# Kernel tuning notes

Hardware: AMD Instinct MI355X
Metric: run time of the kernel (lower is better)

## Reference

```python
import jax, jax.numpy as jnp
import numpy as np

N_NODE = 50000
EMB = 128
LAYERS = 2
B = 1024
L = 50
E = 1_600_000


def setup_inputs() -> dict:
    key = jax.random.key(0)
    ks = jax.random.split(key, 21)
    d = EMB
    stdv = 1.0 / np.sqrt(d)
    u = lambda k, shape: jax.random.uniform(k, shape, minval=-stdv, maxval=stdv, dtype=jnp.float32)
    inp = {
        'adj_row': jax.random.randint(ks[0], (E,), 0, N_NODE, dtype=jnp.int32),
        'adj_col': jax.random.randint(ks[1], (E,), 0, N_NODE, dtype=jnp.int32),
        'adj_val': jax.random.uniform(ks[2], (E,), dtype=jnp.float32) / 32.0,  # ~row-normalized sparse adjacency
        'embedding': jax.random.normal(ks[3], (N_NODE, d), dtype=jnp.float32) * 0.1,
        'session_item': jax.random.randint(ks[4], (B, L), 0, N_NODE, dtype=jnp.int32),  # 0 hits the zero pad row
        'session_len': jnp.full((B, 1), float(L), dtype=jnp.float32),
        'D': jax.random.uniform(ks[5], (B, B), dtype=jnp.float32) / B,
        'A_sess': jax.random.uniform(ks[6], (B, B), dtype=jnp.float32) / B,
        'A_gnn': jax.random.uniform(ks[7], (B, L, 2 * L), dtype=jnp.float32) / L,
        'alias_pos': jax.random.randint(ks[8], (B, L), 0, L, dtype=jnp.int32),
        'hidden': jax.random.normal(ks[9], (B, L, d), dtype=jnp.float32) * 0.1,
        'W_in': u(ks[10], (d, d)), 'b_in': u(ks[11], (d,)),
        'W_out': u(ks[12], (d, d)), 'b_out': u(ks[13], (d,)),
        'w_ih': u(ks[14], (3 * d, 2 * d)), 'b_ih': u(ks[15], (3 * d,)),
        'w_hh': u(ks[16], (3 * d, d)), 'b_hh': u(ks[17], (3 * d,)),
        'b_iah': u(ks[18], (d,)), 'b_oah': u(ks[19], (d,)),
    }
    return inp


def reference(adj_row, adj_col, adj_val, embedding, session_item, session_len,
              D, A_sess, A_gnn, alias_pos, hidden,
              W_in, b_in, W_out, b_out, w_ih, b_ih, w_hh, b_hh, b_iah, b_oah):
    # ---- HyperConv: layers of sparse (COO) adjacency @ embedding, summed over hops ----
    emb = embedding
    final = embedding
    for _ in range(LAYERS):
        emb = jax.ops.segment_sum(adj_val[:, None] * emb[adj_col], adj_row, num_segments=N_NODE)
        final = final + emb
    item_emb = final  # [N_NODE, d]

    # ---- LineConv: zero-padded gather + mean pool over session, then session-graph propagation ----
    pad_table = jnp.concatenate([jnp.zeros((1, EMB), embedding.dtype), embedding], axis=0)
    seq_h = pad_table[session_item]                      # [B, L, d]
    sess = jnp.sum(seq_h, axis=1) / session_len          # [B, d]
    DA = D @ A_sess                                      # [B, B]
    acc = sess
    s = sess
    for _ in range(LAYERS):
        s = DA @ s
        acc = acc + s
    session_emb = acc                                    # [B, d]

    # ---- GNN: gather per-session in/out adjacency rows, gated GRU-style update ----
    in_out = jnp.take_along_axis(A_gnn, alias_pos[:, :, None], axis=1)  # [B, L, 2L]
    h_in = hidden @ W_in.T + b_in
    h_out = hidden @ W_out.T + b_out
    input_in = jnp.einsum('bij,bjd->bid', in_out[:, :, :L], h_in) + b_iah
    input_out = jnp.einsum('bij,bjd->bid', in_out[:, :, L:], h_out) + b_oah
    inputs = jnp.concatenate([input_in, input_out], axis=2)             # [B, L, 2d]
    gi = inputs @ w_ih.T + b_ih
    gh = hidden @ w_hh.T + b_hh
    i_r, i_i, i_n = jnp.split(gi, 3, axis=2)
    h_r, h_i, h_n = jnp.split(gh, 3, axis=2)
    resetgate = jax.nn.sigmoid(i_r + h_r)
    inputgate = jax.nn.sigmoid(i_i + h_i)
    newgate = jnp.tanh(i_n + resetgate * h_n)
    hy = newgate + inputgate * (hidden - newgate)        # [B, L, d]

    return item_emb, session_emb, hy
```

## Files before the change

### kernel.cpp

```cpp
#include <hip/hip_runtime.h>

#define EMB 128
#define NN 50000
#define BB 1024
#define LL 50
#define NBK 49
#define NEB 512
#define NCONV 2048

typedef float f32x4 __attribute__((ext_vector_type(4)));
typedef float f32x2 __attribute__((ext_vector_type(2)));
typedef unsigned short u16;
typedef unsigned int u32;
typedef unsigned long long u64;
typedef u16 u16x4 __attribute__((ext_vector_type(4)));
typedef u32 u32x4 __attribute__((ext_vector_type(4)));
typedef short bf16x8 __attribute__((ext_vector_type(8)));

__device__ __forceinline__ float u2f(u16 u) {
    union { unsigned int i; float f; } v; v.i = ((unsigned int)u) << 16; return v.f;
}
__device__ __forceinline__ u16 f2b(float f) {
    union { float f; unsigned int i; } v; v.f = f;
    unsigned int i = v.i;
    return (u16)((i + 0x7FFFu + ((i >> 16) & 1u)) >> 16);
}
__device__ __forceinline__ float lo2f(u32 w) { return u2f((u16)(w & 0xffffu)); }
__device__ __forceinline__ float hi2f(u32 w) { return u2f((u16)(w >> 16)); }
__device__ __forceinline__ float sigmoidf_(float x) { return 1.f / (1.f + __expf(-x)); }
__device__ __forceinline__ float tanhf_(float x) {
    float e = __expf(-2.f * x);
    return (1.f - e) / (1.f + e);
}

__global__ __launch_bounds__(256) void prep_kernel(
    const float* __restrict__ emb, const float* __restrict__ A, const float* __restrict__ D,
    const float* __restrict__ whh,
    u16* __restrict__ emb_bf, u16* __restrict__ A_bf, u16* __restrict__ D_bf,
    u16* __restrict__ whh_bf,
    const int* __restrict__ rowi, int* __restrict__ bcnt,
    const float* __restrict__ w_ih, const float* __restrict__ W_in, const float* __restrict__ W_out,
    const float* __restrict__ b_in, const float* __restrict__ b_out,
    const float* __restrict__ b_iah, const float* __restrict__ b_oah, const float* __restrict__ b_ih,
    u16* __restrict__ WcT_bf, float* __restrict__ u123,
    int E, int chunk)
{
    __shared__ int lc[NBK];
    __shared__ float wrow[256];
    __shared__ float red[3][256];
    int tid = threadIdx.x;

    if (blockIdx.x >= NCONV) {
        int d = blockIdx.x - NCONV;
        int c = tid;
        wrow[c] = w_ih[d * 256 + c];
        __syncthreads();
        const float* W = (c < 128) ? W_in : W_out;
        const float* wr = wrow + ((c < 128) ? 0 : 128);
        int cc = c & 127;
        float acc = 0.f;
#pragma unroll 4
        for (int j = 0; j < 128; j++) acc += wr[j] * W[j * 128 + cc];
        WcT_bf[d * 256 + c] = f2b(acc);
        float p1 = (c < 128) ? b_in[c] * wrow[c] : 0.f;
        float p2 = (c >= 128) ? b_out[cc] * wrow[c] : 0.f;
        float p3 = (c < 128) ? b_iah[c] * wrow[c] : b_oah[cc] * wrow[c];
        red[0][c] = p1; red[1][c] = p2; red[2][c] = p3;
        __syncthreads();
        for (int off = 128; off > 0; off >>= 1) {
            if (c < off) {
                red[0][c] += red[0][c + off];
                red[1][c] += red[1][c + off];
                red[2][c] += red[2][c + off];
            }
            __syncthreads();
        }
        if (c == 0) {
            u123[d] = red[0][0];
            u123[384 + d] = red[1][0];
            u123[768 + d] = red[2][0] + b_ih[d];
        }
        return;
    }

    int gid = blockIdx.x * 256 + tid;
    int stride = NCONV * 256;
    if (blockIdx.x < NEB) {
        if (tid < NBK) lc[tid] = 0;
        __syncthreads();
        int beg = blockIdx.x * chunk, end = min(E, beg + chunk);
        for (int e = beg + tid; e < end; e += 256)
            atomicAdd(&lc[rowi[e] >> 10], 1);
        __syncthreads();
        if (tid < NBK) bcnt[blockIdx.x * NBK + tid] = lc[tid];
    }
    for (int i = gid; i < 1600000; i += stride) {
        f32x4 v = *(const f32x4*)(emb + (size_t)i * 4);
        u16x4 p;
#pragma unroll
        for (int t = 0; t < 4; t++) p[t] = f2b(v[t]);
        *(u16x4*)(emb_bf + (size_t)i * 4) = p;
    }
    for (int i = gid; i < 2146304; i += stride) {
        const float* s; u16* d; int off;
        if (i < 1048576)      { s = A;   d = A_bf;   off = i; }
        else if (i < 2097152) { s = D;   d = D_bf;   off = i - 1048576; }
        else                  { s = whh; d = whh_bf; off = i - 2097152; }
        d[off] = f2b(s[off]);
    }
}

__global__ __launch_bounds__(512) void bktscan_kernel(
    const int* __restrict__ bcnt, int* __restrict__ sofs, int* __restrict__ btot)
{
    __shared__ int ps[512];
    int k = blockIdx.x, t = threadIdx.x;
    int c = bcnt[t * NBK + k];
    ps[t] = c; __syncthreads();
    for (int off = 1; off < 512; off <<= 1) {
        int v = (t >= off) ? ps[t - off] : 0;
        __syncthreads();
        ps[t] += v; __syncthreads();
    }
    sofs[t * NBK + k] = ps[t] - c;
    if (t == 511) btot[k] = ps[511];
}

__global__ __launch_bounds__(64) void btotal_kernel(
    const int* __restrict__ btot, int* __restrict__ bofs, int E)
{
    if (threadIdx.x == 0) {
        int run = 0;
        for (int k = 0; k < NBK; k++) { bofs[k] = run; run += btot[k]; }
        bofs[NBK] = E;
    }
}

__global__ __launch_bounds__(256) void emit_kernel(
    const int* __restrict__ rowi, const int* __restrict__ coli, const float* __restrict__ val,
    const int* __restrict__ sofs, const int* __restrict__ bofs,
    u64* __restrict__ egs, int E, int chunk)
{
    __shared__ int cur[NBK];
    int b = blockIdx.x, tid = threadIdx.x;
    if (tid < NBK) cur[tid] = bofs[tid] + sofs[b * NBK + tid];
    __syncthreads();
    int beg = b * chunk, end = min(E, beg + chunk);
    for (int e = beg + tid; e < end; e += 256) {
        int r = rowi[e];
        int slot = atomicAdd(&cur[r >> 10], 1);
        u64 entry = ((u64)(u32)(r & 1023) << 32)
                  | (u64)((u32)(u16)coli[e] | ((u32)f2b(val[e]) << 16));
        egs[slot] = entry;
    }
}

__global__ __launch_bounds__(1024) void binsort2_kernel(
    const u64* __restrict__ egs, const int* __restrict__ bofs,
    int* __restrict__ row_ptr, u32* __restrict__ eg, int E)
{
    __shared__ int cnt_s[1024];
    __shared__ int ps[1024];
    int k = blockIdx.x, tid = threadIdx.x;
    int r0 = k << 10;
    int beg = bofs[k], end = bofs[k + 1];
    cnt_s[tid] = 0;
    __syncthreads();
    for (int i = beg + tid; i < end; i += 1024)
        atomicAdd(&cnt_s[(int)(egs[i] >> 32)], 1);
    __syncthreads();
    int v = cnt_s[tid];
    ps[tid] = v; __syncthreads();
    for (int off = 1; off < 1024; off <<= 1) {
        int t = (tid >= off) ? ps[tid - off] : 0;
        __syncthreads();
        ps[tid] += t; __syncthreads();
    }
    int ex = beg + ps[tid] - v;
    if (r0 + tid <= NN) row_ptr[r0 + tid] = ex;
    if (k == NBK - 1 && tid == 1023) row_ptr[NN] = E;
    cnt_s[tid] = ex;
    __syncthreads();
    for (int i = beg + tid; i < end; i += 1024) {
        u64 entry = egs[i];
        int rlo = (int)(entry >> 32);
        int p = atomicAdd(&cnt_s[rlo], 1);
        eg[p] = (u32)entry;
    }
}

template<int FUSE>
__global__ __launch_bounds__(256) void gatherb_kernel(
    const int* __restrict__ row_ptr, const u32* __restrict__ eg,
    const u16* __restrict__ src, const float* __restrict__ emb0,
    u16* __restrict__ dst_bf, float* __restrict__ dst_f)
{
    int wave = threadIdx.x >> 6;
    int lane = threadIdx.x & 63;
    int g  = lane >> 4;
    int fl = lane & 15;
    int r = blockIdx.x * 4 + wave;
    if (r >= NN) return;
    int beg = row_ptr[r], end = row_ptr[r + 1];

    float acc[8];
#pragma unroll
    for (int t = 0; t < 8; t++) acc[t] = 0.f;

    if (beg < end) {
        int last = end - 1;
        int npair = (end - beg + 7) >> 3;
        u32 pkA = eg[min(beg + g, last)];
        u32 pkB = eg[min(beg + 4 + g, last)];
        float vA = (beg + g     < end) ? u2f((u16)(pkA >> 16)) : 0.f;
        float vB = (beg + 4 + g < end) ? u2f((u16)(pkB >> 16)) : 0.f;
        u32x4 xA = *(const u32x4*)(src + ((pkA & 0xffffu) << 7) + (fl << 3));
        u32x4 xB = *(const u32x4*)(src + ((pkB & 0xffffu) << 7) + (fl << 3));
        pkA = eg[min(beg + 8  + g, last)];
        pkB = eg[min(beg + 12 + g, last)];

        int e = beg;
        for (int p = 0; p < npair; p++) {
            float cvA = vA, cvB = vB;
            u32x4 cxA = xA, cxB = xB;
            int eN = e + 8;
            vA = (eN + g     < end) ? u2f((u16)(pkA >> 16)) : 0.f;
            vB = (eN + 4 + g < end) ? u2f((u16)(pkB >> 16)) : 0.f;
            xA = *(const u32x4*)(src + ((pkA & 0xffffu) << 7) + (fl << 3));
            xB = *(const u32x4*)(src + ((pkB & 0xffffu) << 7) + (fl << 3));
            int eS = e + 16;
            pkA = eg[min(eS + g, last)];
            pkB = eg[min(eS + 4 + g, last)];
#pragma unroll
            for (int t = 0; t < 4; t++) {
                acc[2 * t]     += cvA * lo2f(cxA[t]);
                acc[2 * t + 1] += cvA * hi2f(cxA[t]);
            }
#pragma unroll
            for (int t = 0; t < 4; t++) {
                acc[2 * t]     += cvB * lo2f(cxB[t]);
                acc[2 * t + 1] += cvB * hi2f(cxB[t]);
            }
            e += 8;
        }
    }

#pragma unroll
    for (int t = 0; t < 8; t++) {
        acc[t] += __shfl_xor(acc[t], 16);
        acc[t] += __shfl_xor(acc[t], 32);
    }

    if (lane < 16) {
        if (FUSE) {
            u32x4 s = *(const u32x4*)(src + ((u32)r << 7) + (lane << 3));
            const float* e0p = emb0 + ((size_t)r << 7) + (lane << 3);
            f32x4 e0a = *(const f32x4*)e0p;
            f32x4 e0b = *(const f32x4*)(e0p + 4);
            f32x4 o0, o1;
#pragma unroll
            for (int t = 0; t < 2; t++) {
                o0[2 * t]     = acc[2 * t]     + e0a[2 * t]     + lo2f(s[t]);
                o0[2 * t + 1] = acc[2 * t + 1] + e0a[2 * t + 1] + hi2f(s[t]);
                o1[2 * t]     = acc[4 + 2 * t]     + e0b[2 * t]     + lo2f(s[2 + t]);
                o1[2 * t + 1] = acc[4 + 2 * t + 1] + e0b[2 * t + 1] + hi2f(s[2 + t]);
            }
            float* dp = dst_f + ((size_t)r << 7) + (lane << 3);
            *(f32x4*)dp = o0;
            *(f32x4*)(dp + 4) = o1;
        } else {
            u32x4 w;
#pragma unroll
            for (int t = 0; t < 4; t++)
                w[t] = (u32)f2b(acc[2 * t]) | ((u32)f2b(acc[2 * t + 1]) << 16);
            *(u32x4*)(dst_bf + ((size_t)r << 7) + (lane << 3)) = w;
        }
    }
}

__global__ __launch_bounds__(128) void sess_pool_kernel(
    const int* __restrict__ items, const float* __restrict__ emb,
    const float* __restrict__ slen, float* __restrict__ sess, u16* __restrict__ sessT)
{
    int b = blockIdx.x, d = threadIdx.x;
    const int* it = items + b * LL;
    float acc = 0.f;
    for (int l = 0; l < LL; l++) {
        int idx = it[l];
        if (idx > 0) acc += emb[(size_t)(idx - 1) * EMB + d];
    }
    float v = acc / slen[b];
    sess[b * EMB + d] = v;
    sessT[d * BB + b] = f2b(v);
}

template<int WT, int WF>
__global__ __launch_bounds__(256) void mm_mfma_kernel(
    const u16* __restrict__ M_bf, const u16* __restrict__ Xt_bf,
    u16* __restrict__ Ct_bf, float* __restrict__ C_f)
{
    int tid = threadIdx.x;
    int wv = tid >> 6, lane = tid & 63, cl = lane & 15, kg = lane >> 4;
    int rbase = blockIdx.x * 16;
    f32x4 acc[2];
    acc[0] = (f32x4)0.f; acc[1] = (f32x4)0.f;
    const u16* arow = M_bf + (size_t)(rbase + cl) * BB + kg * 8;
    const u16* brow = Xt_bf + (size_t)(wv * 32 + cl) * BB + kg * 8;
#pragma unroll 4
    for (int k0 = 0; k0 < BB; k0 += 32) {
        bf16x8 a  = *(const bf16x8*)(arow + k0);
        bf16x8 b0 = *(const bf16x8*)(brow + k0);
        bf16x8 b1 = *(const bf16x8*)(brow + (size_t)16 * BB + k0);
        acc[0] = __builtin_amdgcn_mfma_f32_16x16x32_bf16(a, b0, acc[0], 0, 0, 0);
        acc[1] = __builtin_amdgcn_mfma_f32_16x16x32_bf16(a, b1, acc[1], 0, 0, 0);
    }
#pragma unroll
    for (int nt = 0; nt < 2; nt++) {
        int col = (wv * 2 + nt) * 16 + cl;
#pragma unroll
        for (int j = 0; j < 4; j++) {
            int row = rbase + kg * 4 + j;
            if (WF) C_f[(size_t)row * EMB + col] = acc[nt][j];
            if (WT) Ct_bf[(size_t)col * BB + row] = f2b(acc[nt][j]);
        }
    }
}

__global__ __launch_bounds__(256) void out1_kernel(
    const float* __restrict__ a, const float* __restrict__ b,
    const float* __restrict__ c, float* __restrict__ o, int n)
{
    int i = blockIdx.x * 256 + threadIdx.x;
    if (i < n) o[i] = a[i] + b[i] + c[i];
}

__global__ __launch_bounds__(512) void gnn_tail_kernel(
    const float* __restrict__ hidden,
    const float* __restrict__ A_gnn, const int* __restrict__ alias_pos,
    const u16* __restrict__ WcT_bf, const u16* __restrict__ w_hh_bf,
    const float* __restrict__ u123, const float* __restrict__ b_hh,
    float* __restrict__ hy)
{
    __shared__ __attribute__((aligned(16))) u16 smem[25600];
    u16* Hs  = smem;
    u16* As  = smem + 8192;
    u16* HsT = smem + 16384;
    u16* M2s = smem + 8192;
    __shared__ float rcs[64][2];

    int b = blockIdx.x;
    int tid = threadIdx.x;
    int wv = tid >> 6, lane = tid & 63, cl = lane & 15, kg = lane >> 4;

    int pr_row[4], pr_c4[4], ppos[4];
#pragma unroll
    for (int it = 0; it < 4; it++) {
        int i = tid + it * 512;
        pr_row[it] = i >> 5; pr_c4[it] = i & 31;
        ppos[it] = (pr_row[it] < LL) ? alias_pos[b * LL + pr_row[it]] : 0;
    }
    float av[4][4];
#pragma unroll
    for (int it = 0; it < 4; it++) {
        const float* ar = A_gnn + ((size_t)b * LL + ppos[it]) * (2 * LL);
#pragma unroll
        for (int t = 0; t < 4; t++) {
            int jp = pr_c4[it] * 4 + t;
            int col = (jp < 64) ? jp : (50 + (jp - 64));
            int ok = (pr_row[it] < LL) && ((jp < 64) ? (jp < LL) : ((jp - 64) < LL));
            av[it][t] = ok ? ar[col] : 0.f;
        }
    }
    const float* hsrc = hidden + (size_t)b * LL * EMB;
    f32x4 hv[4]; int hrow[4], hc4[4];
#pragma unroll
    for (int i2 = 0; i2 < 4; i2++) {
        int lin = i2 * 512 + tid;
        hrow[i2] = lin >> 5; hc4[i2] = lin & 31;
        hv[i2] = (hrow[i2] < LL) ? *(const f32x4*)(hsrc + hrow[i2] * 128 + hc4[i2] * 4) : (f32x4)0.f;
    }
#pragma unroll
    for (int it = 0; it < 4; it++) {
        u16x4 p;
#pragma unroll
        for (int t = 0; t < 4; t++) p[t] = f2b(av[it][t]);
        *(u16x4*)((char*)As + pr_row[it] * 256 + ((pr_c4[it] * 8) ^ ((pr_row[it] & 7) << 4))) = p;
    }
#pragma unroll
    for (int i2 = 0; i2 < 4; i2++) {
        u16x4 q;
#pragma unroll
        for (int t = 0; t < 4; t++) q[t] = f2b(hv[i2][t]);
        *(u16x4*)((char*)Hs + hrow[i2] * 256 + ((hc4[i2] * 8) ^ ((hrow[i2] & 7) << 4))) = q;
    }
#pragma unroll
    for (int i2 = 0; i2 < 4; i2++) {
        int idx = i2 * 512 + tid;
        int c = idx & 127, rg = idx >> 7;
        int r0 = rg * 4;
        u16x4 p = (u16x4)0;
#pragma unroll
        for (int k = 0; k < 4; k++) {
            int row = r0 + k;
            p[k] = (row < LL) ? f2b(hsrc[row * 128 + c]) : (u16)0;
        }
        *(u16x4*)&HsT[c * 72 + r0] = p;
    }
    __syncthreads();

    if (tid < 128) {
        int row = tid >> 1, half = tid & 1;
        float s = 0.f;
#pragma unroll
        for (int c4 = 0; c4 < 16; c4++) {
            u16x4 v = *(const u16x4*)((const char*)As + row * 256 +
                        ((half * 128 + c4 * 8) ^ ((row & 7) << 4)));
            s += u2f(v[0]) + u2f(v[1]) + u2f(v[2]) + u2f(v[3]);
        }
        rcs[row][half] = s;
    }

    {
        int h = wv >> 2, ct = wv & 3;
        f32x4 m2acc[4][2];
#pragma unroll
        for (int mt = 0; mt < 4; mt++) { m2acc[mt][0] = (f32x4)0.f; m2acc[mt][1] = (f32x4)0.f; }
#pragma unroll
        for (int ks = 0; ks < 2; ks++) {
            bf16x8 bb[2];
#pragma unroll
            for (int nt = 0; nt < 2; nt++) {
                int c = ct * 32 + nt * 16 + cl;
                bb[nt] = *(const bf16x8*)&HsT[c * 72 + ks * 32 + kg * 8];
            }
#pragma unroll
            for (int mt = 0; mt < 4; mt++) {
                int mr = mt * 16 + cl;
                bf16x8 aa = *(const bf16x8*)((const char*)As + mr * 256 +
                             ((h * 128 + ks * 64 + kg * 16) ^ ((mr & 7) << 4)));
#pragma unroll
                for (int nt = 0; nt < 2; nt++)
                    m2acc[mt][nt] = __builtin_amdgcn_mfma_f32_16x16x32_bf16(aa, bb[nt], m2acc[mt][nt], 0, 0, 0);
            }
        }
        __syncthreads();
#pragma unroll
        for (int mt = 0; mt < 4; mt++)
#pragma unroll
            for (int nt = 0; nt < 2; nt++) {
                int kcol = h * 128 + ct * 32 + nt * 16 + cl;
#pragma unroll
                for (int j = 0; j < 4; j++) {
                    int row = mt * 16 + kg * 4 + j;
                    *(u16*)((char*)M2s + row * 512 + ((kcol * 2) ^ ((row & 7) << 4))) =
                        f2b(m2acc[mt][nt][j]);
                }
            }
    }
    __syncthreads();

    f32x4 acc_ri[4][2];
    f32x4 acc_n1[4];
    f32x4 acc_n2[4];
#pragma unroll
    for (int mt = 0; mt < 4; mt++) {
        acc_ri[mt][0] = (f32x4)0.f; acc_ri[mt][1] = (f32x4)0.f;
        acc_n1[mt] = (f32x4)0.f; acc_n2[mt] = (f32x4)0.f;
    }

#pragma unroll
    for (int ks = 0; ks < 8; ks++) {
        bf16x8 a[4];
#pragma unroll
        for (int mt = 0; mt < 4; mt++) {
            int mr = mt * 16 + cl;
            a[mt] = *(const bf16x8*)((const char*)M2s + mr * 512 +
                     ((ks * 64 + kg * 16) ^ ((mr & 7) << 4)));
        }
#pragma unroll
        for (int g = 0; g < 3; g++) {
            int brow = g * 128 + wv * 16 + cl;
            bf16x8 bw = *(const bf16x8*)(WcT_bf + (size_t)brow * 256 + ks * 32 + kg * 8);
#pragma unroll
            for (int mt = 0; mt < 4; mt++) {
                f32x4* dst = (g < 2) ? &acc_ri[mt][g] : &acc_n1[mt];
                *dst = __builtin_amdgcn_mfma_f32_16x16x32_bf16(a[mt], bw, *dst, 0, 0, 0);
            }
        }
    }
#pragma unroll
    for (int ks = 0; ks < 4; ks++) {
        bf16x8 a[4];
#pragma unroll
        for (int mt = 0; mt < 4; mt++) {
            int mr = mt * 16 + cl;
            a[mt] = *(const bf16x8*)((const char*)Hs + mr * 256 +
                     ((ks * 64 + kg * 16) ^ ((mr & 7) << 4)));
        }
#pragma unroll
        for (int g = 0; g < 3; g++) {
            int brow = g * 128 + wv * 16 + cl;
            bf16x8 bw = *(const bf16x8*)(w_hh_bf + (size_t)brow * 128 + ks * 32 + kg * 8);
#pragma unroll
            for (int mt = 0; mt < 4; mt++) {
                f32x4* dst = (g < 2) ? &acc_ri[mt][g] : &acc_n2[mt];
                *dst = __builtin_amdgcn_mfma_f32_16x16x32_bf16(a[mt], bw, *dst, 0, 0, 0);
            }
        }
    }

    {
        int d = wv * 16 + cl;
        float brh = b_hh[d], bih_ = b_hh[128 + d], bnh = b_hh[256 + d];
        float u1r = u123[d],       u1i = u123[128 + d],       u1n = u123[256 + d];
        float u2r = u123[384 + d], u2i = u123[384 + 128 + d], u2n = u123[384 + 256 + d];
        float u3r = u123[768 + d], u3i = u123[768 + 128 + d], u3n = u123[768 + 256 + d];
#pragma unroll
        for (int mt = 0; mt < 4; mt++)
#pragma unroll
            for (int j = 0; j < 4; j++) {
                int row = mt * 16 + kg * 4 + j;
                if (row >= LL) continue;
                float cr = rcs[row][0], dr = rcs[row][1];
                float pr  = acc_ri[mt][0][j] + cr * u1r + dr * u2r + u3r + brh;
                float pi  = acc_ri[mt][1][j] + cr * u1i + dr * u2i + u3i + bih_;
                float pn1 = acc_n1[mt][j]    + cr * u1n + dr * u2n + u3n;
                float pn2 = acc_n2[mt][j] + bnh;
                float rg = sigmoidf_(pr);
                float ig = sigmoidf_(pi);
                float ng = tanhf_(pn1 + rg * pn2);
                u16 hb = *(const u16*)((const char*)Hs + row * 256 + ((d * 2) ^ ((row & 7) << 4)));
                float h = u2f(hb);
                hy[((size_t)b * LL + row) * 128 + d] = ng + ig * (h - ng);
            }
    }
}

extern "C" void kernel_launch(void* const* d_in, const int* in_sizes, int n_in,
                              void* d_out, int out_size, void* d_ws, size_t ws_size,
                              hipStream_t stream) {
    (void)n_in; (void)out_size; (void)ws_size;
    const int*   adj_row      = (const int*)d_in[0];
    const int*   adj_col      = (const int*)d_in[1];
    const float* adj_val      = (const float*)d_in[2];
    const float* embedding    = (const float*)d_in[3];
    const int*   session_item = (const int*)d_in[4];
    const float* session_len  = (const float*)d_in[5];
    const float* Dm           = (const float*)d_in[6];
    const float* A_sess       = (const float*)d_in[7];
    const float* A_gnn        = (const float*)d_in[8];
    const int*   alias_pos    = (const int*)d_in[9];
    const float* hidden       = (const float*)d_in[10];
    const float* W_in         = (const float*)d_in[11];
    const float* b_in         = (const float*)d_in[12];
    const float* W_out        = (const float*)d_in[13];
    const float* b_out        = (const float*)d_in[14];
    const float* w_ih         = (const float*)d_in[15];
    const float* b_ih         = (const float*)d_in[16];
    const float* w_hh         = (const float*)d_in[17];
    const float* b_hh         = (const float*)d_in[18];
    const float* b_iah        = (const float*)d_in[19];
    const float* b_oah        = (const float*)d_in[20];
    const int E = in_sizes[0];

    float* out0 = (float*)d_out;
    float* out1 = out0 + 6400000;
    float* out2 = out1 + 131072;

    float* ws = (float*)d_ws;
    u16*  emb_bf  = (u16*)ws;
    int*  bcnt  = (int*)(ws + 3200000);
    int*  sofs  = (int*)(ws + 3230000);
    int*  btot  = (int*)(ws + 3260000);
    u16*  accA_bf = (u16*)(ws + 3200000);
    u32*  eg    = (u32*)(ws + 6400000);
    u64*  egs   = (u64*)(ws + 8000000);
    float* sess  = ws + 11200000;
    u16*   sessT = (u16*)(ws + 11350000);
    u16*   t1T   = (u16*)(ws + 11400000);
    u16*   s1T   = (u16*)(ws + 11450000);
    u16*   t2T   = (u16*)(ws + 11500000);
    float* s1    = ws + 11550000;
    float* s2    = ws + 11700000;
    u16*   A_bf  = (u16*)(ws + 11850000);
    u16*   D_bf  = (u16*)(ws + 12400000);
    int*   row_ptr = (int*)(ws + 12950000);
    int*   bofs    = row_ptr + NN + 1;
    u16* WcT_bf    = (u16*)(ws + 13107200);
    u16* w_hh_bf   = WcT_bf + 98304;
    float* u123    = (float*)(w_hh_bf + 49152);

    int chunk = (E + NEB - 1) / NEB;

    prep_kernel<<<NCONV + 384, 256, 0, stream>>>(embedding, A_sess, Dm, w_hh,
                                          emb_bf, A_bf, D_bf, w_hh_bf,
                                          adj_row, bcnt,
                                          w_ih, W_in, W_out, b_in, b_out, b_iah, b_oah, b_ih,
                                          WcT_bf, u123,
                                          E, chunk);

    bktscan_kernel<<<NBK, 512, 0, stream>>>(bcnt, sofs, btot);
    btotal_kernel<<<1, 64, 0, stream>>>(btot, bofs, E);
    emit_kernel<<<NEB, 256, 0, stream>>>(adj_row, adj_col, adj_val, sofs, bofs, egs, E, chunk);
    binsort2_kernel<<<NBK, 1024, 0, stream>>>(egs, bofs, row_ptr, eg, E);
    gatherb_kernel<0><<<(NN + 3) / 4, 256, 0, stream>>>(row_ptr, eg, emb_bf, embedding, accA_bf, (float*)nullptr);
    gatherb_kernel<1><<<(NN + 3) / 4, 256, 0, stream>>>(row_ptr, eg, accA_bf, embedding, (u16*)nullptr, out0);

    sess_pool_kernel<<<BB, 128, 0, stream>>>(session_item, embedding, session_len, sess, sessT);
    mm_mfma_kernel<1, 0><<<64, 256, 0, stream>>>(A_bf, sessT, t1T, (float*)nullptr);
    mm_mfma_kernel<1, 1><<<64, 256, 0, stream>>>(D_bf, t1T, s1T, s1);
    mm_mfma_kernel<1, 0><<<64, 256, 0, stream>>>(A_bf, s1T, t2T, (float*)nullptr);
    mm_mfma_kernel<0, 1><<<64, 256, 0, stream>>>(D_bf, t2T, (u16*)nullptr, s2);
    out1_kernel<<<(131072 + 255) / 256, 256, 0, stream>>>(sess, s1, s2, out1, 131072);

    gnn_tail_kernel<<<BB, 512, 0, stream>>>(hidden, A_gnn, alias_pos,
                                            WcT_bf, w_hh_bf, u123, b_hh, out2);
}
```

Baseline: 314.8 us.

## Split GNN tail kernel into two half-column blocks per session

The GNN tail kernel now launches two 256-thread blocks per session instead of one 512-thread block. Each block computes only half of the output hidden dimensions in the GRU gate GEMMs. Both blocks still load the A_gnn rows and hidden, and each recomputes the full M2 product (A × hidden) in shared memory. The aim is more blocks in flight and smaller blocks for better occupancy and scheduling. The cost is duplicated global loads, bf16 conversions and the M2 product, plus more registers per thread for the doubled accumulators.

```diff
diff --git a/kernel.cpp b/kernel.cpp
--- a/kernel.cpp
+++ b/kernel.cpp
@@ -334,7 +334,7 @@
     if (i < n) o[i] = a[i] + b[i] + c[i];
 }
 
-__global__ __launch_bounds__(512) void gnn_tail_kernel(
+__global__ __launch_bounds__(256) void gnn_tail_kernel(
     const float* __restrict__ hidden,
     const float* __restrict__ A_gnn, const int* __restrict__ alias_pos,
     const u16* __restrict__ WcT_bf, const u16* __restrict__ w_hh_bf,
@@ -348,20 +348,21 @@
     u16* M2s = smem + 8192;
     __shared__ float rcs[64][2];
 
-    int b = blockIdx.x;
+    int b    = blockIdx.x & 1023;
+    int half = blockIdx.x >> 10;
     int tid = threadIdx.x;
     int wv = tid >> 6, lane = tid & 63, cl = lane & 15, kg = lane >> 4;
 
-    int pr_row[4], pr_c4[4], ppos[4];
-#pragma unroll
-    for (int it = 0; it < 4; it++) {
-        int i = tid + it * 512;
+    int pr_row[8], pr_c4[8], ppos[8];
+#pragma unroll
+    for (int it = 0; it < 8; it++) {
+        int i = tid + it * 256;
         pr_row[it] = i >> 5; pr_c4[it] = i & 31;
         ppos[it] = (pr_row[it] < LL) ? alias_pos[b * LL + pr_row[it]] : 0;
     }
-    float av[4][4];
-#pragma unroll
-    for (int it = 0; it < 4; it++) {
+    float av[8][4];
+#pragma unroll
+    for (int it = 0; it < 8; it++) {
         const float* ar = A_gnn + ((size_t)b * LL + ppos[it]) * (2 * LL);
 #pragma unroll
         for (int t = 0; t < 4; t++) {
@@ -371,31 +372,27 @@
             av[it][t] = ok ? ar[col] : 0.f;
         }
     }
-    const float* hsrc = hidden + (size_t)b * LL * EMB;
-    f32x4 hv[4]; int hrow[4], hc4[4];
-#pragma unroll
-    for (int i2 = 0; i2 < 4; i2++) {
-        int lin = i2 * 512 + tid;
-        hrow[i2] = lin >> 5; hc4[i2] = lin & 31;
-        hv[i2] = (hrow[i2] < LL) ? *(const f32x4*)(hsrc + hrow[i2] * 128 + hc4[i2] * 4) : (f32x4)0.f;
-    }
-#pragma unroll
-    for (int it = 0; it < 4; it++) {
+#pragma unroll
+    for (int it = 0; it < 8; it++) {
         u16x4 p;
 #pragma unroll
         for (int t = 0; t < 4; t++) p[t] = f2b(av[it][t]);
         *(u16x4*)((char*)As + pr_row[it] * 256 + ((pr_c4[it] * 8) ^ ((pr_row[it] & 7) << 4))) = p;
     }
-#pragma unroll
-    for (int i2 = 0; i2 < 4; i2++) {
+    const float* hsrc = hidden + (size_t)b * LL * EMB;
+#pragma unroll
+    for (int i2 = 0; i2 < 8; i2++) {
+        int lin = i2 * 256 + tid;
+        int hrow = lin >> 5, hc4 = lin & 31;
+        f32x4 v = (hrow < LL) ? *(const f32x4*)(hsrc + hrow * 128 + hc4 * 4) : (f32x4)0.f;
         u16x4 q;
 #pragma unroll
-        for (int t = 0; t < 4; t++) q[t] = f2b(hv[i2][t]);
-        *(u16x4*)((char*)Hs + hrow[i2] * 256 + ((hc4[i2] * 8) ^ ((hrow[i2] & 7) << 4))) = q;
-    }
-#pragma unroll
-    for (int i2 = 0; i2 < 4; i2++) {
-        int idx = i2 * 512 + tid;
+        for (int t = 0; t < 4; t++) q[t] = f2b(v[t]);
+        *(u16x4*)((char*)Hs + hrow * 256 + ((hc4 * 8) ^ ((hrow & 7) << 4))) = q;
+    }
+#pragma unroll
+    for (int i2 = 0; i2 < 8; i2++) {
+        int idx = i2 * 256 + tid;
         int c = idx & 127, rg = idx >> 7;
         int r0 = rg * 4;
         u16x4 p = (u16x4)0;
@@ -409,22 +406,24 @@
     __syncthreads();
 
     if (tid < 128) {
-        int row = tid >> 1, half = tid & 1;
+        int row = tid >> 1, hf = tid & 1;
         float s = 0.f;
 #pragma unroll
         for (int c4 = 0; c4 < 16; c4++) {
             u16x4 v = *(const u16x4*)((const char*)As + row * 256 +
-                        ((half * 128 + c4 * 8) ^ ((row & 7) << 4)));
+                        ((hf * 128 + c4 * 8) ^ ((row & 7) << 4)));
             s += u2f(v[0]) + u2f(v[1]) + u2f(v[2]) + u2f(v[3]);
         }
-        rcs[row][half] = s;
+        rcs[row][hf] = s;
     }
 
     {
-        int h = wv >> 2, ct = wv & 3;
-        f32x4 m2acc[4][2];
-#pragma unroll
-        for (int mt = 0; mt < 4; mt++) { m2acc[mt][0] = (f32x4)0.f; m2acc[mt][1] = (f32x4)0.f; }
+        int ct = wv;
+        f32x4 m2acc[2][4][2];
+#pragma unroll
+        for (int h = 0; h < 2; h++)
+#pragma unroll
+            for (int mt = 0; mt < 4; mt++) { m2acc[h][mt][0] = (f32x4)0.f; m2acc[h][mt][1] = (f32x4)0.f; }
 #pragma unroll
         for (int ks = 0; ks < 2; ks++) {
             bf16x8 bb[2];
@@ -434,31 +433,36 @@
                 bb[nt] = *(const bf16x8*)&HsT[c * 72 + ks * 32 + kg * 8];
             }
 #pragma unroll
-            for (int mt = 0; mt < 4; mt++) {
-                int mr = mt * 16 + cl;
-                bf16x8 aa = *(const bf16x8*)((const char*)As + mr * 256 +
-                             ((h * 128 + ks * 64 + kg * 16) ^ ((mr & 7) << 4)));
-#pragma unroll
-                for (int nt = 0; nt < 2; nt++)
-                    m2acc[mt][nt] = __builtin_amdgcn_mfma_f32_16x16x32_bf16(aa, bb[nt], m2acc[mt][nt], 0, 0, 0);
-            }
+            for (int h = 0; h < 2; h++)
+#pragma unroll
+                for (int mt = 0; mt < 4; mt++) {
+                    int mr = mt * 16 + cl;
+                    bf16x8 aa = *(const bf16x8*)((const char*)As + mr * 256 +
+                                 ((h * 128 + ks * 64 + kg * 16) ^ ((mr & 7) << 4)));
+#pragma unroll
+                    for (int nt = 0; nt < 2; nt++)
+                        m2acc[h][mt][nt] = __builtin_amdgcn_mfma_f32_16x16x32_bf16(aa, bb[nt], m2acc[h][mt][nt], 0, 0, 0);
+                }
         }
         __syncthreads();
 #pragma unroll
-        for (int mt = 0; mt < 4; mt++)
-#pragma unroll
-            for (int nt = 0; nt < 2; nt++) {
-                int kcol = h * 128 + ct * 32 + nt * 16 + cl;
-#pragma unroll
-                for (int j = 0; j < 4; j++) {
-                    int row = mt * 16 + kg * 4 + j;
-                    *(u16*)((char*)M2s + row * 512 + ((kcol * 2) ^ ((row & 7) << 4))) =
-                        f2b(m2acc[mt][nt][j]);
+        for (int h = 0; h < 2; h++)
+#pragma unroll
+            for (int mt = 0; mt < 4; mt++)
+#pragma unroll
+                for (int nt = 0; nt < 2; nt++) {
+                    int kcol = h * 128 + ct * 32 + nt * 16 + cl;
+#pragma unroll
+                    for (int j = 0; j < 4; j++) {
+                        int row = mt * 16 + kg * 4 + j;
+                        *(u16*)((char*)M2s + row * 512 + ((kcol * 2) ^ ((row & 7) << 4))) =
+                            f2b(m2acc[h][mt][nt][j]);
+                    }
                 }
-            }
     }
     __syncthreads();
 
+    int dl = half * 64 + wv * 16 + cl;
     f32x4 acc_ri[4][2];
     f32x4 acc_n1[4];
     f32x4 acc_n2[4];
@@ -479,7 +483,7 @@
         }
 #pragma unroll
         for (int g = 0; g < 3; g++) {
-            int brow = g * 128 + wv * 16 + cl;
+            int brow = g * 128 + dl;
             bf16x8 bw = *(const bf16x8*)(WcT_bf + (size_t)brow * 256 + ks * 32 + kg * 8);
 #pragma unroll
             for (int mt = 0; mt < 4; mt++) {
@@ -499,7 +503,7 @@
         }
 #pragma unroll
         for (int g = 0; g < 3; g++) {
-            int brow = g * 128 + wv * 16 + cl;
+            int brow = g * 128 + dl;
             bf16x8 bw = *(const bf16x8*)(w_hh_bf + (size_t)brow * 128 + ks * 32 + kg * 8);
 #pragma unroll
             for (int mt = 0; mt < 4; mt++) {
@@ -510,7 +514,7 @@
     }
 
     {
-        int d = wv * 16 + cl;
+        int d = dl;
         float brh = b_hh[d], bih_ = b_hh[128 + d], bnh = b_hh[256 + d];
         float u1r = u123[d],       u1i = u123[128 + d],       u1n = u123[256 + d];
         float u2r = u123[384 + d], u2i = u123[384 + 128 + d], u2n = u123[384 + 256 + d];
@@ -613,6 +617,6 @@
     mm_mfma_kernel<0, 1><<<64, 256, 0, stream>>>(D_bf, t2T, (u16*)nullptr, s2);
     out1_kernel<<<(131072 + 255) / 256, 256, 0, stream>>>(sess, s1, s2, out1, 131072);
 
-    gnn_tail_kernel<<<BB, 512, 0, stream>>>(hidden, A_gnn, alias_pos,
-                                            WcT_bf, w_hh_bf, u123, b_hh, out2);
-}
+    gnn_tail_kernel<<<2 * BB, 256, 0, stream>>>(hidden, A_gnn, alias_pos,
+                                                WcT_bf, w_hh_bf, u123, b_hh, out2);
+}
```

Result: slower. 326.4 us (+3.7%).
